# Kernel tuning notes

Measured on AMD Instinct MI355X. Metric: run time of the kernel, lower is better.

Reference implementation:

```python
import jax, jax.numpy as jnp
import numpy as np

B, S, D, H = 4, 2048, 512, 8
DK = D // H


def setup_inputs() -> dict:
    key = jax.random.key(0)
    ks = jax.random.split(key, 11)
    scale = 1.0 / np.sqrt(D)
    inp = {
        'q': jax.random.normal(ks[0], (B, S, D), jnp.float32),
        'k': jax.random.normal(ks[1], (B, S, D), jnp.float32),
        'v': jax.random.normal(ks[2], (B, S, D), jnp.float32),
        'mask': jnp.tril(jnp.ones((S, S), jnp.int32))[None, None, :, :],  # [1,1,S,S] causal
        'w_q': jax.random.normal(ks[3], (D, D), jnp.float32) * scale,
        'b_q': jnp.zeros((D,), jnp.float32),
        'w_k': jax.random.normal(ks[4], (D, D), jnp.float32) * scale,
        'b_k': jnp.zeros((D,), jnp.float32),
        'w_v': jax.random.normal(ks[5], (D, D), jnp.float32) * scale,
        'b_v': jnp.zeros((D,), jnp.float32),
        'w_o': jax.random.normal(ks[6], (D, D), jnp.float32) * scale,
        'b_o': jnp.zeros((D,), jnp.float32),
    }
    return inp


def reference(q, k, v, mask, w_q, b_q, w_k, b_k, w_v, b_v, w_o, b_o):
    # QKV projections (nn.Linear: x @ W^T + b)
    def split_heads(x):  # [B,S,D] -> [B,H,S,DK]
        return x.reshape(B, S, H, DK).transpose(0, 2, 1, 3)

    qh = split_heads(q @ w_q.T + b_q)
    kh = split_heads(k @ w_k.T + b_k)
    vh = split_heads(v @ w_v.T + b_v)

    scores = jnp.einsum('bhqd,bhkd->bhqk', qh, kh) / jnp.sqrt(jnp.float32(DK))
    scores = jnp.where(mask == 0, jnp.float32(-1e9), scores)
    attn = jax.nn.softmax(scores, axis=-1)  # dropout is identity in eval
    ctx = jnp.einsum('bhqk,bhkd->bhqd', attn, vh)  # [B,H,S,DK]
    ctx = ctx.transpose(0, 2, 1, 3).reshape(B, S, D)
    return ctx @ w_o.T + b_o
```

## Files before the change

kernel.cpp:

```cpp
#include <hip/hip_runtime.h>
#include <hip/hip_bf16.h>


#define BATCH  4
#define SLEN   2048
#define DMODEL 512
#define NHEAD  8
#define DHEAD  64
#define MROWS  (BATCH * SLEN)

#define NQ ((size_t)MROWS * DMODEL)
#define NW ((size_t)DMODEL * DMODEL)
#define NB ((size_t)DMODEL)
#define CVT_TOTAL (3 * NQ + 4 * NW + 4 * NB)

#define SCALE_L2E 0.180336880f

typedef short bf16x8 __attribute__((ext_vector_type(8)));
typedef float f32x4  __attribute__((ext_vector_type(4)));

typedef unsigned int __attribute__((address_space(1))) glb_u32_t;
typedef unsigned int __attribute__((address_space(3))) lds_u32_t;

__device__ __forceinline__ void async_copy16(const unsigned short* g, unsigned short* l) {
    __builtin_amdgcn_global_load_lds((glb_u32_t*)g, (lds_u32_t*)l, 16, 0, 0);
}

__device__ __forceinline__ float bf2f(unsigned short u) {
    union { unsigned int i; float f; } v; v.i = ((unsigned int)u) << 16; return v.f;
}
__device__ __forceinline__ unsigned short f2bf(float f) {
    union { float f; unsigned int i; } v; v.f = f;
    unsigned int x = v.i;
    return (unsigned short)((x + 0x7fffu + ((x >> 16) & 1u)) >> 16);
}
__device__ __forceinline__ unsigned int pkbf(float a, float b) {
    union { __hip_bfloat162 h; unsigned int u; } cv;
    cv.h = __float22bfloat162_rn(float2{a, b});
    return cv.u;
}

__device__ __forceinline__ void wait0_barrier() {
    asm volatile("s_waitcnt vmcnt(0)" ::: "memory");
    __builtin_amdgcn_s_barrier();
    asm volatile("" ::: "memory");
}

__global__ __launch_bounds__(256)
void cvt_kernel(const float* __restrict__ q, const float* __restrict__ k,
                const float* __restrict__ v,
                const float* __restrict__ wq, const float* __restrict__ wk,
                const float* __restrict__ wv, const float* __restrict__ wo,
                const float* __restrict__ bq, const float* __restrict__ bk,
                const float* __restrict__ bv, const float* __restrict__ bo,
                unsigned short* __restrict__ dst)
{
    const size_t i4 = ((size_t)blockIdx.x * 256 + threadIdx.x) * 4;
    if (i4 >= CVT_TOTAL) return;
    const float* src;
    size_t off;
    if      (i4 <     NQ)          { src = q;  off = i4; }
    else if (i4 < 2 * NQ)          { src = k;  off = i4 - NQ; }
    else if (i4 < 3 * NQ)          { src = v;  off = i4 - 2 * NQ; }
    else if (i4 < 3 * NQ + NW)     { src = wq; off = i4 - 3 * NQ; }
    else if (i4 < 3 * NQ + 2 * NW) { src = wk; off = i4 - 3 * NQ - NW; }
    else if (i4 < 3 * NQ + 3 * NW) { src = wv; off = i4 - 3 * NQ - 2 * NW; }
    else if (i4 < 3 * NQ + 4 * NW) { src = wo; off = i4 - 3 * NQ - 3 * NW; }
    else if (i4 < 3 * NQ + 4 * NW + NB)     { src = bq; off = i4 - 3 * NQ - 4 * NW; }
    else if (i4 < 3 * NQ + 4 * NW + 2 * NB) { src = bk; off = i4 - 3 * NQ - 4 * NW - NB; }
    else if (i4 < 3 * NQ + 4 * NW + 3 * NB) { src = bv; off = i4 - 3 * NQ - 4 * NW - 2 * NB; }
    else                                    { src = bo; off = i4 - 3 * NQ - 4 * NW - 3 * NB; }
    const float4 f = *(const float4*)(src + off);
    ushort4 o;
    o.x = f2bf(f.x); o.y = f2bf(f.y); o.z = f2bf(f.z); o.w = f2bf(f.w);
    *(ushort4*)(dst + i4) = o;
}

template <typename OutT>
__device__ __forceinline__ void gemm_body(const unsigned short* __restrict__ A,
                                          const unsigned short* __restrict__ W,
                                          const unsigned short* __restrict__ bias,
                                          OutT* __restrict__ C, int mode)
{
    __shared__ __align__(16) unsigned short As[2][128 * 32];
    __shared__ __align__(16) unsigned short Bs[2][128 * 32];

    const int tid  = threadIdx.x;
    const int wave = tid >> 6;
    const int lane = tid & 63;
    const int l15  = lane & 15;
    const int quad = lane >> 4;
    const int m0   = blockIdx.x * 128;
    const int n0   = blockIdx.y * 128;
    const int wm   = (wave & 1) * 64;
    const int wn   = (wave >> 1) * 64;
    const int srow = lane >> 2;
    const int scol = (((lane & 3) ^ (srow & 3)) * 8);
    const int rsw  = (quad ^ (l15 & 3)) * 8;

    auto stage = [&](int k0, int buf) {
        async_copy16(A + (size_t)(m0 + wave * 16 + srow) * DMODEL + k0 + scol, As[buf] + wave * 512);
        async_copy16(A + (size_t)(m0 + (wave + 4) * 16 + srow) * DMODEL + k0 + scol, As[buf] + (wave + 4) * 512);
        async_copy16(W + (size_t)(n0 + wave * 16 + srow) * DMODEL + k0 + scol, Bs[buf] + wave * 512);
        async_copy16(W + (size_t)(n0 + (wave + 4) * 16 + srow) * DMODEL + k0 + scol, Bs[buf] + (wave + 4) * 512);
    };

    f32x4 acc[4][4] = {};
    stage(0, 0);

    #pragma unroll 1
    for (int kt = 0; kt < 16; kt++) {
        const int cur = kt & 1;
        wait0_barrier();
        if (kt < 15) stage((kt + 1) * 32, cur ^ 1);

        bf16x8 af[4], bfr[4];
        #pragma unroll
        for (int i = 0; i < 4; i++)
            af[i] = *(const bf16x8*)(As[cur] + (wm + i * 16 + l15) * 32 + rsw);
        #pragma unroll
        for (int j = 0; j < 4; j++)
            bfr[j] = *(const bf16x8*)(Bs[cur] + (wn + j * 16 + l15) * 32 + rsw);
        #pragma unroll
        for (int i = 0; i < 4; i++)
            #pragma unroll
            for (int j = 0; j < 4; j++)
                acc[i][j] = __builtin_amdgcn_mfma_f32_16x16x32_bf16(af[i], bfr[j], acc[i][j], 0, 0, 0);
    }

    if (mode == 2) {
        #pragma unroll
        for (int j = 0; j < 4; j++) {
            const int col = n0 + wn + j * 16 + l15;
            const float bv = bf2f(bias[col]);
            const int hh = col >> 6, dk = col & 63;
            #pragma unroll
            for (int i = 0; i < 4; i++) {
                const int row = m0 + wm + i * 16 + quad * 4;
                const int bb = row >> 11, s = row & 2047;
                uint2 o2;
                o2.x = pkbf(acc[i][j][0] + bv, acc[i][j][1] + bv);
                o2.y = pkbf(acc[i][j][2] + bv, acc[i][j][3] + bv);
                *(uint2*)((unsigned short*)C + ((size_t)((bb * NHEAD + hh) * DHEAD + dk)) * SLEN + s) = o2;
            }
        }
    } else {
        const float oscale = (mode == 0) ? SCALE_L2E : 1.0f;
        #pragma unroll
        for (int j = 0; j < 4; j++) {
            const int col = n0 + wn + j * 16 + l15;
            const float bv = bf2f(bias[col]);
            #pragma unroll
            for (int i = 0; i < 4; i++) {
                const int row = m0 + wm + i * 16 + quad * 4;
                #pragma unroll
                for (int r = 0; r < 4; r++) {
                    const float val = (acc[i][j][r] + bv) * oscale;
                    if constexpr (sizeof(OutT) == 4)
                        C[(size_t)(row + r) * DMODEL + col] = val;
                    else
                        C[(size_t)(row + r) * DMODEL + col] = f2bf(val);
                }
            }
        }
    }
}

__global__ __launch_bounds__(256, 3)
void qkv_gemm_kernel(const unsigned short* __restrict__ qin,
                     const unsigned short* __restrict__ kin,
                     const unsigned short* __restrict__ vin,
                     const unsigned short* __restrict__ wq,
                     const unsigned short* __restrict__ bq,
                     const unsigned short* __restrict__ wk,
                     const unsigned short* __restrict__ bk,
                     const unsigned short* __restrict__ wv,
                     const unsigned short* __restrict__ bv,
                     unsigned short* __restrict__ qh,
                     unsigned short* __restrict__ kh,
                     unsigned short* __restrict__ vt)
{
    const int z = blockIdx.z;
    const unsigned short* A    = (z == 0) ? qin : (z == 1) ? kin : vin;
    const unsigned short* W    = (z == 0) ? wq  : (z == 1) ? wk  : wv;
    const unsigned short* bias = (z == 0) ? bq  : (z == 1) ? bk  : bv;
    unsigned short*       C    = (z == 0) ? qh  : (z == 1) ? kh  : vt;
    gemm_body<unsigned short>(A, W, bias, C, z);
}

__global__ __launch_bounds__(256, 3)
void oproj_gemm_kernel(const unsigned short* __restrict__ ctx,
                       const unsigned short* __restrict__ wo,
                       const unsigned short* __restrict__ bo,
                       float* __restrict__ out)
{
    gemm_body<float>(ctx, wo, bo, out, 3);
}

__global__ __launch_bounds__(256, 4)
void attn_kernel(const unsigned short* __restrict__ qh,
                 const unsigned short* __restrict__ kh,
                 const unsigned short* __restrict__ vt,
                 unsigned short* __restrict__ ctx)
{
    __shared__ __align__(16) unsigned short Ks[2][64 * 64];
    __shared__ __align__(16) unsigned short Vs[2][64 * 64];
    __shared__ __align__(16) unsigned short Ps[4 * 16 * 64];

    const int tid  = threadIdx.x;
    const int wave = tid >> 6;
    const int lane = tid & 63;
    const int l15  = lane & 15;
    const int quad = lane >> 4;

    const int bh = blockIdx.x;
    const int x  = blockIdx.y;
    const int qt = (x & 1) ? (x >> 1) : (31 - (x >> 1));
    const int b  = bh >> 3;
    const int h  = bh & 7;

    const size_t base = (size_t)b * SLEN * DMODEL + (size_t)h * DHEAD;
    const unsigned short* Q  = qh + base;
    const unsigned short* K  = kh + base;
    const unsigned short* VT = vt + (size_t)bh * DHEAD * SLEN;

    const int krow_l = lane >> 3;
    const int kcol_l = ((lane & 7) ^ (krow_l & 7)) * 8;

    const int qrow = qt * 64 + wave * 16 + l15;
    bf16x8 qf0 = *(const bf16x8*)(Q + (size_t)qrow * DMODEL + quad * 8);
    bf16x8 qf1 = *(const bf16x8*)(Q + (size_t)qrow * DMODEL + 32 + quad * 8);

    f32x4 oacc[4] = {};
    float lsum = 0.0f;

    unsigned short* Pw = Ps + wave * (16 * 64);
    const int ktiles = qt + 1;

    auto stageKV = [&](int kt, int buf) {
        async_copy16(K + (size_t)(kt * 64 + wave * 8 + krow_l) * DMODEL + kcol_l,
                     Ks[buf] + wave * 512);
        async_copy16(K + (size_t)(kt * 64 + (wave + 4) * 8 + krow_l) * DMODEL + kcol_l,
                     Ks[buf] + (wave + 4) * 512);
        async_copy16(VT + (size_t)(wave * 8 + krow_l) * SLEN + kt * 64 + kcol_l,
                     Vs[buf] + wave * 512);
        async_copy16(VT + (size_t)((wave + 4) * 8 + krow_l) * SLEN + kt * 64 + kcol_l,
                     Vs[buf] + (wave + 4) * 512);
    };

    stageKV(0, 0);

    #pragma unroll 1
    for (int kt = 0; kt < ktiles; kt++) {
        const int cur = kt & 1;
        wait0_barrier();
        if (kt + 1 < ktiles) stageKV(kt + 1, cur ^ 1);

        f32x4 sacc[4] = {};
        #pragma unroll
        for (int kk = 0; kk < 2; kk++) {
            const bf16x8 qf = kk ? qf1 : qf0;
            #pragma unroll
            for (int j = 0; j < 4; j++) {
                bf16x8 kf = *(const bf16x8*)(Ks[cur] + (j * 16 + l15) * 64
                                                + (((kk * 4 + quad) ^ (l15 & 7)) * 8));
                sacc[j] = __builtin_amdgcn_mfma_f32_16x16x32_bf16(kf, qf, sacc[j], 0, 0, 0);
            }
        }

        if (kt == qt) {
            #pragma unroll
            for (int j = 0; j < 4; j++)
                #pragma unroll
                for (int r = 0; r < 4; r++) {
                    const int kv = kt * 64 + j * 16 + quad * 4 + r;
                    if (kv > qrow) sacc[j][r] = -1e30f;
                }
        }

        #pragma unroll
        for (int j = 0; j < 4; j++) {
            const float p0 = exp2f(sacc[j][0]);
            const float p1 = exp2f(sacc[j][1]);
            const float p2v = exp2f(sacc[j][2]);
            const float p3 = exp2f(sacc[j][3]);
            lsum += (p0 + p1) + (p2v + p3);
            uint2 pw;
            pw.x = pkbf(p0, p1);
            pw.y = pkbf(p2v, p3);
            const int chunk = (j * 2 + (quad >> 1)) ^ (l15 & 7);
            *(uint2*)(Pw + l15 * 64 + chunk * 8 + (quad & 1) * 4) = pw;
        }
        asm volatile("s_waitcnt lgkmcnt(0)" ::: "memory");

        #pragma unroll
        for (int kk = 0; kk < 2; kk++) {
            bf16x8 pf = *(const bf16x8*)(Pw + l15 * 64 + (((kk * 4 + quad) ^ (l15 & 7)) * 8));
            #pragma unroll
            for (int jd = 0; jd < 4; jd++) {
                bf16x8 vf = *(const bf16x8*)(Vs[cur] + (jd * 16 + l15) * 64
                                                + (((kk * 4 + quad) ^ (l15 & 7)) * 8));
                oacc[jd] = __builtin_amdgcn_mfma_f32_16x16x32_bf16(vf, pf, oacc[jd], 0, 0, 0);
            }
        }
    }

    lsum += __shfl_xor(lsum, 16, 64);
    lsum += __shfl_xor(lsum, 32, 64);
    const float invl = 1.0f / lsum;

    #pragma unroll
    for (int jd = 0; jd < 4; jd++) {
        uint2 o2;
        o2.x = pkbf(oacc[jd][0] * invl, oacc[jd][1] * invl);
        o2.y = pkbf(oacc[jd][2] * invl, oacc[jd][3] * invl);
        *(uint2*)(ctx + base + (size_t)qrow * DMODEL + jd * 16 + quad * 4) = o2;
    }
}

extern "C" void kernel_launch(void* const* d_in, const int* in_sizes, int n_in,
                              void* d_out, int out_size, void* d_ws, size_t ws_size,
                              hipStream_t stream)
{
    const float* q   = (const float*)d_in[0];
    const float* k   = (const float*)d_in[1];
    const float* v   = (const float*)d_in[2];
    const float* w_q = (const float*)d_in[4];
    const float* b_q = (const float*)d_in[5];
    const float* w_k = (const float*)d_in[6];
    const float* b_k = (const float*)d_in[7];
    const float* w_v = (const float*)d_in[8];
    const float* b_v = (const float*)d_in[9];
    const float* w_o = (const float*)d_in[10];
    const float* b_o = (const float*)d_in[11];
    float* out = (float*)d_out;

    unsigned short* ws = (unsigned short*)d_ws;
    unsigned short* qb  = ws;
    unsigned short* kb  = ws + NQ;
    unsigned short* vb  = ws + 2 * NQ;
    unsigned short* wqb = ws + 3 * NQ;
    unsigned short* wkb = wqb + NW;
    unsigned short* wvb = wkb + NW;
    unsigned short* wob = wvb + NW;
    unsigned short* bqb = wob + NW;
    unsigned short* bkb = bqb + NB;
    unsigned short* bvb = bkb + NB;
    unsigned short* bob = bvb + NB;
    unsigned short* qh  = bob + NB;
    unsigned short* kh  = qh + NQ;
    unsigned short* vt  = kh + NQ;
    unsigned short* ctx = vt + NQ;

    dim3 blk(256);
    hipLaunchKernelGGL(cvt_kernel, dim3((unsigned)(CVT_TOTAL / 4 / 256)), blk, 0, stream,
                       q, k, v, w_q, w_k, w_v, w_o, b_q, b_k, b_v, b_o, ws);
    hipLaunchKernelGGL(qkv_gemm_kernel, dim3(MROWS / 128, DMODEL / 128, 3), blk, 0, stream,
                       qb, kb, vb, wqb, bqb, wkb, bkb, wvb, bvb, qh, kh, vt);
    hipLaunchKernelGGL(attn_kernel, dim3(BATCH * NHEAD, 32), blk, 0, stream,
                       qh, kh, vt, ctx);
    hipLaunchKernelGGL(oproj_gemm_kernel, dim3(MROWS / 128, DMODEL / 128), blk, 0, stream,
                       ctx, wob, bob, out);
}
```

Baseline: 204.6 us.

## Run attention with one wave per 64-row query tile and drop barriers

The attention kernel now runs one 64-lane wave per block, and that wave handles all four 16-row query sub-tiles. K and V fragments loaded from LDS are reused across the four sub-tiles, and block barriers are replaced by vmcnt waits. The query-tile ordering changes to a four-way zigzag to balance causal work. The cost is many more accumulator registers (launch_bounds 64,1) and only one wave per block with 40KB of LDS. That may limit occupancy and latency hiding, and the wave must now issue every K/V copy itself.

```diff
diff --git a/kernel.cpp b/kernel.cpp
--- a/kernel.cpp
+++ b/kernel.cpp
@@ -197,7 +197,7 @@
     gemm_body<float>(ctx, wo, bo, out, 3);
 }
 
-__global__ __launch_bounds__(256, 4)
+__global__ __launch_bounds__(64, 1)
 void attn_kernel(const unsigned short* __restrict__ qh,
                  const unsigned short* __restrict__ kh,
                  const unsigned short* __restrict__ vt,
@@ -205,19 +205,19 @@
 {
     __shared__ __align__(16) unsigned short Ks[2][64 * 64];
     __shared__ __align__(16) unsigned short Vs[2][64 * 64];
-    __shared__ __align__(16) unsigned short Ps[4 * 16 * 64];
-
-    const int tid  = threadIdx.x;
-    const int wave = tid >> 6;
-    const int lane = tid & 63;
+    __shared__ __align__(16) unsigned short Ps[64 * 64];
+
+    const int lane = threadIdx.x & 63;
     const int l15  = lane & 15;
     const int quad = lane >> 4;
 
     const int bh = blockIdx.x;
     const int x  = blockIdx.y;
-    const int qt = (x & 1) ? (x >> 1) : (31 - (x >> 1));
+    const int g  = x & 7, s = x >> 3;
+    const int qt = (s == 0) ? g : (s == 1) ? 15 - g : (s == 2) ? 16 + g : 31 - g;
     const int b  = bh >> 3;
     const int h  = bh & 7;
+    const int q0 = qt * 64;
 
     const size_t base = (size_t)b * SLEN * DMODEL + (size_t)h * DHEAD;
     const unsigned short* Q  = qh + base;
@@ -227,25 +227,27 @@
     const int krow_l = lane >> 3;
     const int kcol_l = ((lane & 7) ^ (krow_l & 7)) * 8;
 
-    const int qrow = qt * 64 + wave * 16 + l15;
-    bf16x8 qf0 = *(const bf16x8*)(Q + (size_t)qrow * DMODEL + quad * 8);
-    bf16x8 qf1 = *(const bf16x8*)(Q + (size_t)qrow * DMODEL + 32 + quad * 8);
-
-    f32x4 oacc[4] = {};
-    float lsum = 0.0f;
-
-    unsigned short* Pw = Ps + wave * (16 * 64);
+    bf16x8 qf[4][2];
+    #pragma unroll
+    for (int i = 0; i < 4; i++)
+        #pragma unroll
+        for (int kk = 0; kk < 2; kk++)
+            qf[i][kk] = *(const bf16x8*)(Q + (size_t)(q0 + i * 16 + l15) * DMODEL
+                                           + kk * 32 + quad * 8);
+
+    f32x4 oacc[4][4] = {};
+    float lsum[4] = {0.f, 0.f, 0.f, 0.f};
+
     const int ktiles = qt + 1;
 
     auto stageKV = [&](int kt, int buf) {
-        async_copy16(K + (size_t)(kt * 64 + wave * 8 + krow_l) * DMODEL + kcol_l,
-                     Ks[buf] + wave * 512);
-        async_copy16(K + (size_t)(kt * 64 + (wave + 4) * 8 + krow_l) * DMODEL + kcol_l,
-                     Ks[buf] + (wave + 4) * 512);
-        async_copy16(VT + (size_t)(wave * 8 + krow_l) * SLEN + kt * 64 + kcol_l,
-                     Vs[buf] + wave * 512);
-        async_copy16(VT + (size_t)((wave + 4) * 8 + krow_l) * SLEN + kt * 64 + kcol_l,
-                     Vs[buf] + (wave + 4) * 512);
+        #pragma unroll
+        for (int c = 0; c < 8; c++) {
+            async_copy16(K + (size_t)(kt * 64 + c * 8 + krow_l) * DMODEL + kcol_l,
+                         Ks[buf] + c * 512);
+            async_copy16(VT + (size_t)(c * 8 + krow_l) * SLEN + kt * 64 + kcol_l,
+                         Vs[buf] + c * 512);
+        }
     };
 
     stageKV(0, 0);
@@ -253,68 +255,89 @@
     #pragma unroll 1
     for (int kt = 0; kt < ktiles; kt++) {
         const int cur = kt & 1;
-        wait0_barrier();
-        if (kt + 1 < ktiles) stageKV(kt + 1, cur ^ 1);
-
-        f32x4 sacc[4] = {};
+        if (kt + 1 < ktiles) {
+            stageKV(kt + 1, cur ^ 1);
+            asm volatile("s_waitcnt vmcnt(16)" ::: "memory");
+        } else {
+            asm volatile("s_waitcnt vmcnt(0)" ::: "memory");
+        }
+
+        f32x4 sacc[4][4] = {};
         #pragma unroll
         for (int kk = 0; kk < 2; kk++) {
-            const bf16x8 qf = kk ? qf1 : qf0;
             #pragma unroll
             for (int j = 0; j < 4; j++) {
                 bf16x8 kf = *(const bf16x8*)(Ks[cur] + (j * 16 + l15) * 64
                                                 + (((kk * 4 + quad) ^ (l15 & 7)) * 8));
-                sacc[j] = __builtin_amdgcn_mfma_f32_16x16x32_bf16(kf, qf, sacc[j], 0, 0, 0);
+                #pragma unroll
+                for (int i = 0; i < 4; i++)
+                    sacc[i][j] = __builtin_amdgcn_mfma_f32_16x16x32_bf16(kf, qf[i][kk], sacc[i][j], 0, 0, 0);
             }
         }
 
         if (kt == qt) {
             #pragma unroll
-            for (int j = 0; j < 4; j++)
+            for (int i = 0; i < 4; i++) {
+                const int qrow = q0 + i * 16 + l15;
                 #pragma unroll
-                for (int r = 0; r < 4; r++) {
-                    const int kv = kt * 64 + j * 16 + quad * 4 + r;
-                    if (kv > qrow) sacc[j][r] = -1e30f;
-                }
-        }
-
-        #pragma unroll
-        for (int j = 0; j < 4; j++) {
-            const float p0 = exp2f(sacc[j][0]);
-            const float p1 = exp2f(sacc[j][1]);
-            const float p2v = exp2f(sacc[j][2]);
-            const float p3 = exp2f(sacc[j][3]);
-            lsum += (p0 + p1) + (p2v + p3);
-            uint2 pw;
-            pw.x = pkbf(p0, p1);
-            pw.y = pkbf(p2v, p3);
-            const int chunk = (j * 2 + (quad >> 1)) ^ (l15 & 7);
-            *(uint2*)(Pw + l15 * 64 + chunk * 8 + (quad & 1) * 4) = pw;
-        }
+                for (int j = 0; j < 4; j++)
+                    #pragma unroll
+                    for (int r = 0; r < 4; r++) {
+                        const int kv = kt * 64 + j * 16 + quad * 4 + r;
+                        if (kv > qrow) sacc[i][j][r] = -1e30f;
+                    }
+            }
+        }
+
+        #pragma unroll
+        for (int i = 0; i < 4; i++)
+            #pragma unroll
+            for (int j = 0; j < 4; j++) {
+                const float p0 = exp2f(sacc[i][j][0]);
+                const float p1 = exp2f(sacc[i][j][1]);
+                const float p2v = exp2f(sacc[i][j][2]);
+                const float p3 = exp2f(sacc[i][j][3]);
+                lsum[i] += (p0 + p1) + (p2v + p3);
+                uint2 pw;
+                pw.x = pkbf(p0, p1);
+                pw.y = pkbf(p2v, p3);
+                const int chunk = (j * 2 + (quad >> 1)) ^ (l15 & 7);
+                *(uint2*)(Ps + (i * 16 + l15) * 64 + chunk * 8 + (quad & 1) * 4) = pw;
+            }
         asm volatile("s_waitcnt lgkmcnt(0)" ::: "memory");
 
         #pragma unroll
         for (int kk = 0; kk < 2; kk++) {
-            bf16x8 pf = *(const bf16x8*)(Pw + l15 * 64 + (((kk * 4 + quad) ^ (l15 & 7)) * 8));
-            #pragma unroll
-            for (int jd = 0; jd < 4; jd++) {
-                bf16x8 vf = *(const bf16x8*)(Vs[cur] + (jd * 16 + l15) * 64
+            bf16x8 vf[4];
+            #pragma unroll
+            for (int jd = 0; jd < 4; jd++)
+                vf[jd] = *(const bf16x8*)(Vs[cur] + (jd * 16 + l15) * 64
                                                 + (((kk * 4 + quad) ^ (l15 & 7)) * 8));
-                oacc[jd] = __builtin_amdgcn_mfma_f32_16x16x32_bf16(vf, pf, oacc[jd], 0, 0, 0);
+            #pragma unroll
+            for (int i = 0; i < 4; i++) {
+                bf16x8 pf = *(const bf16x8*)(Ps + (i * 16 + l15) * 64
+                                                + (((kk * 4 + quad) ^ (l15 & 7)) * 8));
+                #pragma unroll
+                for (int jd = 0; jd < 4; jd++)
+                    oacc[i][jd] = __builtin_amdgcn_mfma_f32_16x16x32_bf16(vf[jd], pf, oacc[i][jd], 0, 0, 0);
             }
         }
     }
 
-    lsum += __shfl_xor(lsum, 16, 64);
-    lsum += __shfl_xor(lsum, 32, 64);
-    const float invl = 1.0f / lsum;
-
     #pragma unroll
-    for (int jd = 0; jd < 4; jd++) {
-        uint2 o2;
-        o2.x = pkbf(oacc[jd][0] * invl, oacc[jd][1] * invl);
-        o2.y = pkbf(oacc[jd][2] * invl, oacc[jd][3] * invl);
-        *(uint2*)(ctx + base + (size_t)qrow * DMODEL + jd * 16 + quad * 4) = o2;
+    for (int i = 0; i < 4; i++) {
+        float l = lsum[i];
+        l += __shfl_xor(l, 16, 64);
+        l += __shfl_xor(l, 32, 64);
+        const float invl = 1.0f / l;
+        const int qrow = q0 + i * 16 + l15;
+        #pragma unroll
+        for (int jd = 0; jd < 4; jd++) {
+            uint2 o2;
+            o2.x = pkbf(oacc[i][jd][0] * invl, oacc[i][jd][1] * invl);
+            o2.y = pkbf(oacc[i][jd][2] * invl, oacc[i][jd][3] * invl);
+            *(uint2*)(ctx + base + (size_t)qrow * DMODEL + jd * 16 + quad * 4) = o2;
+        }
     }
 }
 
@@ -357,7 +380,7 @@
                        q, k, v, w_q, w_k, w_v, w_o, b_q, b_k, b_v, b_o, ws);
     hipLaunchKernelGGL(qkv_gemm_kernel, dim3(MROWS / 128, DMODEL / 128, 3), blk, 0, stream,
                        qb, kb, vb, wqb, bqb, wkb, bkb, wvb, bvb, qh, kh, vt);
-    hipLaunchKernelGGL(attn_kernel, dim3(BATCH * NHEAD, 32), blk, 0, stream,
+    hipLaunchKernelGGL(attn_kernel, dim3(BATCH * NHEAD, 32), dim3(64), 0, stream,
                        qh, kh, vt, ctx);
     hipLaunchKernelGGL(oproj_gemm_kernel, dim3(MROWS / 128, DMODEL / 128), blk, 0, stream,
                        ctx, wob, bob, out);
```

New measurement: 242.3 us. +18.4%, slower.
